# Kernel optimization log

Hardware: AMD Instinct MI355X
Metric: run time of the kernel (lower is better)

The kernel has to match this reference:

```python
import jax, jax.numpy as jnp
import numpy as np

D_MODEL = 1024
NUM_HEADS = 16
HEAD_DIM = D_MODEL // NUM_HEADS
WINDOW = 16
DILATION = 3
SCALE = HEAD_DIM ** -0.5


def _linear(x, W, b):
    # torch nn.Linear: y = x @ W.T + b, W: [out, in]
    return x @ W.T + b


def _chunk_attention(x, Wq, bq, Wk, bk, Wv, bv, chunk):
    B, L, D = x.shape
    pad = (-L) % chunk
    if pad:
        x = jnp.pad(x, ((0, 0), (0, pad), (0, 0)))
    Lp = L + pad
    nC = Lp // chunk
    xr = x.reshape(B * nC, chunk, D)  # [BC, c, D]

    def heads(t):
        return t.reshape(B * nC, chunk, NUM_HEADS, HEAD_DIM).transpose(0, 2, 1, 3)

    q = heads(_linear(xr, Wq, bq))  # [BC, H, c, hd]
    k = heads(_linear(xr, Wk, bk))
    v = heads(_linear(xr, Wv, bv))
    attn = jax.nn.softmax(jnp.einsum('bhqd,bhkd->bhqk', q, k) * SCALE, axis=-1)
    out = jnp.einsum('bhqk,bhkd->bhqd', attn, v)  # [BC, H, c, hd]
    out = out.transpose(0, 2, 1, 3).reshape(B, Lp, D)
    return out[:, :L, :]


def setup_inputs() -> dict:
    key = jax.random.key(0)
    ks = jax.random.split(key, 9)
    s = 1.0 / np.sqrt(D_MODEL)
    x = jax.random.normal(ks[0], (4, 4096, D_MODEL), dtype=jnp.float32)
    def lin(kw, kb):
        W = jax.random.uniform(kw, (D_MODEL, D_MODEL), minval=-s, maxval=s, dtype=jnp.float32)
        b = jax.random.uniform(kb, (D_MODEL,), minval=-s, maxval=s, dtype=jnp.float32)
        return W, b
    Wq, bq = lin(ks[1], ks[2])
    Wk, bk = lin(ks[3], ks[4])
    Wv, bv = lin(ks[5], ks[6])
    Wo, bo = lin(ks[7], ks[8])
    return {"x": x, "Wq": Wq, "bq": bq, "Wk": Wk, "bk": bk,
            "Wv": Wv, "bv": bv, "Wo": Wo, "bo": bo}


def reference(x, Wq, bq, Wk, bk, Wv, bv, Wo, bo):
    B, L, D = x.shape
    # local windowed attention
    local_out = _chunk_attention(x, Wq, bq, Wk, bk, Wv, bv, WINDOW)
    # dilated (atrous) attention: stride-DILATION interleave via reshape/permute
    pad = (-L) % DILATION
    x_pad = jnp.pad(x, ((0, 0), (0, pad), (0, 0))) if pad else x
    Lp = L + pad
    xv = x_pad.reshape(B, Lp // DILATION, DILATION, D).transpose(0, 2, 1, 3)
    x_atrous = xv.reshape(B * DILATION, Lp // DILATION, D)
    a = _chunk_attention(x_atrous, Wq, bq, Wk, bk, Wv, bv, WINDOW)
    a = a.reshape(B, DILATION, Lp // DILATION, D).transpose(0, 2, 1, 3).reshape(B, Lp, D)
    atrous_out = a[:, :L, :]
    return _linear(local_out + atrous_out, Wo, bo)
```

## Files before the change

kernel.cpp:

```cpp
#include <hip/hip_runtime.h>
#include <hip/hip_bf16.h>
#include <stdint.h>

typedef unsigned short ushort_t;
typedef __attribute__((ext_vector_type(8))) short bf16x8;
typedef __attribute__((ext_vector_type(4))) float f32x4;

__device__ __forceinline__ ushort_t f2bf(float f) {
    uint32_t u = __builtin_bit_cast(uint32_t, f);
    u += 0x7FFF + ((u >> 16) & 1);
    return (ushort_t)(u >> 16);
}
__device__ __forceinline__ float bf2f(ushort_t h) {
    return __builtin_bit_cast(float, (uint32_t)h << 16);
}

__device__ __forceinline__ f32x4 mfma16(bf16x8 a, bf16x8 b, f32x4 c) {
    return __builtin_amdgcn_mfma_f32_16x16x32_bf16(a, b, c, 0, 0, 0);
}

#define GLL(g, l) __builtin_amdgcn_global_load_lds(                              \
    (const __attribute__((address_space(1))) void*)(g),                          \
    (__attribute__((address_space(3))) void*)(l), 16, 0, 0)


__global__ __launch_bounds__(256) void cvt_f32_to_bf16(
    const float* __restrict__ src, ushort_t* __restrict__ dst, int n8)
{
    int i = blockIdx.x * blockDim.x + threadIdx.x;
    if (i >= n8) return;
    const float4* s = (const float4*)src + (size_t)i * 2;
    float4 a = s[0], b = s[1];
    union { bf16x8 v; ushort_t u[8]; } o;
    o.u[0] = f2bf(a.x); o.u[1] = f2bf(a.y); o.u[2] = f2bf(a.z); o.u[3] = f2bf(a.w);
    o.u[4] = f2bf(b.x); o.u[5] = f2bf(b.y); o.u[6] = f2bf(b.z); o.u[7] = f2bf(b.w);
    *(bf16x8*)(dst + (size_t)i * 8) = o.v;
}

__global__ __launch_bounds__(256) void pack_bias(
    const float* __restrict__ bq, const float* __restrict__ bk,
    const float* __restrict__ bv, float* __restrict__ dst)
{
    int i = blockIdx.x * blockDim.x + threadIdx.x;
    float v = (i < 1024) ? bq[i] : (i < 2048 ? bk[i - 1024] : bv[i - 2048]);
    dst[i] = v;
}


template<int MODE>
__global__ __launch_bounds__(256) void gemm_bt(
    const ushort_t* __restrict__ A, const ushort_t* __restrict__ B,
    const float* __restrict__ bias, void* __restrict__ outp,
    int M, int K)
{
    __shared__ ushort_t As[128 * 32];
    __shared__ ushort_t Bs[128 * 32];
    const int t = threadIdx.x;
    const int wave = t >> 6, lane = t & 63;
    const int m0 = blockIdx.x * 128;
    const int n0 = blockIdx.y * 128;
    const int wr = wave >> 1, wc = wave & 1;
    const int lg = lane >> 4, ln = lane & 15;

    f32x4 acc[4][4];
#pragma unroll
    for (int i = 0; i < 4; ++i)
#pragma unroll
        for (int j = 0; j < 4; ++j) acc[i][j] = (f32x4){0.f, 0.f, 0.f, 0.f};

    for (int k0 = 0; k0 < K; k0 += 32) {
#pragma unroll
        for (int i = 0; i < 2; ++i) {
            int chunk = i * 256 + t;
            int row = chunk >> 2, kc = chunk & 3;
            const ushort_t* ga = A + (size_t)(m0 + row) * K + (k0 + kc * 8);
            GLL(ga, (char*)As + (i * 256 + wave * 64) * 16);
            const ushort_t* gb = B + (size_t)(n0 + row) * K + (k0 + kc * 8);
            GLL(gb, (char*)Bs + (i * 256 + wave * 64) * 16);
        }
        __syncthreads();
        bf16x8 af[4], bfr[4];
#pragma unroll
        for (int mi = 0; mi < 4; ++mi)
            af[mi] = *(const bf16x8*)&As[(wr * 64 + mi * 16 + ln) * 32 + lg * 8];
#pragma unroll
        for (int ni = 0; ni < 4; ++ni)
            bfr[ni] = *(const bf16x8*)&Bs[(wc * 64 + ni * 16 + ln) * 32 + lg * 8];
#pragma unroll
        for (int mi = 0; mi < 4; ++mi)
#pragma unroll
            for (int ni = 0; ni < 4; ++ni)
                acc[mi][ni] = mfma16(af[mi], bfr[ni], acc[mi][ni]);
        __syncthreads();
    }

#pragma unroll
    for (int mi = 0; mi < 4; ++mi) {
#pragma unroll
        for (int ni = 0; ni < 4; ++ni) {
            int n = n0 + wc * 64 + ni * 16 + ln;
            float bval = bias[n];
#pragma unroll
            for (int r = 0; r < 4; ++r) {
                int m = m0 + wr * 64 + mi * 16 + lg * 4 + r;
                float v = acc[mi][ni][r] + bval;
                if (MODE == 0) {
                    int which = n >> 10, col = n & 1023;
                    ushort_t* o = (ushort_t*)outp + (size_t)which * ((size_t)M * 1024)
                                  + (size_t)m * 1024 + col;
                    *o = f2bf(v);
                } else {
                    ((float*)outp)[(size_t)m * 1024 + n] = v;
                }
            }
        }
    }
}


__device__ __forceinline__ bf16x8 bias8(const float* __restrict__ b, int off) {
    float4 f0 = *(const float4*)(b + off);
    float4 f1 = *(const float4*)(b + off + 4);
    union { bf16x8 v; ushort_t u[8]; } o;
    o.u[0] = f2bf(f0.x); o.u[1] = f2bf(f0.y); o.u[2] = f2bf(f0.z); o.u[3] = f2bf(f0.w);
    o.u[4] = f2bf(f1.x); o.u[5] = f2bf(f1.y); o.u[6] = f2bf(f1.z); o.u[7] = f2bf(f1.w);
    return o.v;
}


__global__ __launch_bounds__(64) void attn_local(
    const ushort_t* __restrict__ Q, const ushort_t* __restrict__ K,
    const ushort_t* __restrict__ V, ushort_t* __restrict__ S)
{
    const int bid = blockIdx.x;
    const int h = bid & 15;
    const int c = bid >> 4;
    const int lane = threadIdx.x;
    const int g = lane >> 4, nn = lane & 15;
    __shared__ ushort_t lds_p[16 * 16];
    __shared__ ushort_t vt[64 * 16];

    const size_t rowb = (size_t)c * 16;
    size_t aoff = (rowb + nn) * 1024 + h * 64 + g * 8;
    bf16x8 qa0 = *(const bf16x8*)(Q + aoff);
    bf16x8 qa1 = *(const bf16x8*)(Q + aoff + 32);
    bf16x8 kb0 = *(const bf16x8*)(K + aoff);
    bf16x8 kb1 = *(const bf16x8*)(K + aoff + 32);
    f32x4 sc = {0.f, 0.f, 0.f, 0.f};
    sc = mfma16(qa0, kb0, sc);
    sc = mfma16(qa1, kb1, sc);

#pragma unroll
    for (int r = 0; r < 4; ++r) {
        float s = sc[r] * 0.125f;
        float mx = s;
#pragma unroll
        for (int off = 1; off < 16; off <<= 1) mx = fmaxf(mx, __shfl_xor(mx, off, 64));
        float e = __expf(s - mx);
        float sm = e;
#pragma unroll
        for (int off = 1; off < 16; off <<= 1) sm += __shfl_xor(sm, off, 64);
        lds_p[(g * 4 + r) * 16 + nn] = f2bf(e / sm);
    }

#pragma unroll
    for (int it = 0; it < 2; ++it) {
        int u = it * 64 + lane;
        int n = u >> 3, cc = u & 7;
        bf16x8 vv = *(const bf16x8*)(V + (rowb + n) * 1024 + h * 64 + cc * 8);
        union { bf16x8 v; ushort_t u8[8]; } vu; vu.v = vv;
#pragma unroll
        for (int j = 0; j < 8; ++j) vt[(cc * 8 + j) * 16 + n] = vu.u8[j];
    }
    __syncthreads();

    bf16x8 zero8 = {};
    bf16x8 pa = (g < 2) ? *(const bf16x8*)&lds_p[nn * 16 + g * 8] : zero8;
#pragma unroll
    for (int dt = 0; dt < 4; ++dt) {
        bf16x8 vb = (g < 2) ? *(const bf16x8*)&vt[(dt * 16 + nn) * 16 + g * 8] : zero8;
        f32x4 o = mfma16(pa, vb, (f32x4){0.f, 0.f, 0.f, 0.f});
#pragma unroll
        for (int r = 0; r < 4; ++r) {
            size_t orow = rowb + g * 4 + r;
            S[orow * 1024 + h * 64 + dt * 16 + nn] = f2bf(o[r]);
        }
    }
}


__global__ __launch_bounds__(64) void attn_atrous(
    const ushort_t* __restrict__ Q, const ushort_t* __restrict__ K,
    const ushort_t* __restrict__ V,
    const float* __restrict__ bq, const float* __restrict__ bk,
    const float* __restrict__ bv, ushort_t* __restrict__ S)
{
    const int bid = blockIdx.x;
    const int h = bid & 15;
    const int tmp = bid >> 4;
    const int c = tmp % 86;
    const int sidx = tmp / 86;
    const int b = sidx / 3, dil = sidx % 3;
    const int lane = threadIdx.x;
    const int g = lane >> 4, nn = lane & 15;
    __shared__ ushort_t lds_p[16 * 16];
    __shared__ ushort_t vt[64 * 16];

    const int dof = h * 64 + g * 8;
    const int p_n = 3 * (c * 16 + nn) + dil;
    bf16x8 qa0, qa1, kb0, kb1;
    if (p_n < 4096) {
        size_t o = ((size_t)b * 4096 + p_n) * 1024 + dof;
        qa0 = *(const bf16x8*)(Q + o);
        qa1 = *(const bf16x8*)(Q + o + 32);
        kb0 = *(const bf16x8*)(K + o);
        kb1 = *(const bf16x8*)(K + o + 32);
    } else {
        qa0 = bias8(bq, dof); qa1 = bias8(bq, dof + 32);
        kb0 = bias8(bk, dof); kb1 = bias8(bk, dof + 32);
    }
    f32x4 sc = {0.f, 0.f, 0.f, 0.f};
    sc = mfma16(qa0, kb0, sc);
    sc = mfma16(qa1, kb1, sc);

#pragma unroll
    for (int r = 0; r < 4; ++r) {
        float s = sc[r] * 0.125f;
        float mx = s;
#pragma unroll
        for (int off = 1; off < 16; off <<= 1) mx = fmaxf(mx, __shfl_xor(mx, off, 64));
        float e = __expf(s - mx);
        float sm = e;
#pragma unroll
        for (int off = 1; off < 16; off <<= 1) sm += __shfl_xor(sm, off, 64);
        lds_p[(g * 4 + r) * 16 + nn] = f2bf(e / sm);
    }

#pragma unroll
    for (int it = 0; it < 2; ++it) {
        int u = it * 64 + lane;
        int n = u >> 3, cc = u & 7;
        int p_v = 3 * (c * 16 + n) + dil;
        bf16x8 vv = (p_v < 4096)
            ? *(const bf16x8*)(V + ((size_t)b * 4096 + p_v) * 1024 + h * 64 + cc * 8)
            : bias8(bv, h * 64 + cc * 8);
        union { bf16x8 v; ushort_t u8[8]; } vu; vu.v = vv;
#pragma unroll
        for (int j = 0; j < 8; ++j) vt[(cc * 8 + j) * 16 + n] = vu.u8[j];
    }
    __syncthreads();

    bf16x8 zero8 = {};
    bf16x8 pa = (g < 2) ? *(const bf16x8*)&lds_p[nn * 16 + g * 8] : zero8;
#pragma unroll
    for (int dt = 0; dt < 4; ++dt) {
        bf16x8 vb = (g < 2) ? *(const bf16x8*)&vt[(dt * 16 + nn) * 16 + g * 8] : zero8;
        f32x4 o = mfma16(pa, vb, (f32x4){0.f, 0.f, 0.f, 0.f});
#pragma unroll
        for (int r = 0; r < 4; ++r) {
            int p_q = 3 * (c * 16 + g * 4 + r) + dil;
            if (p_q < 4096) {
                size_t off = ((size_t)b * 4096 + p_q) * 1024 + h * 64 + dt * 16 + nn;
                S[off] = f2bf(bf2f(S[off]) + o[r]);
            }
        }
    }
}


extern "C" void kernel_launch(void* const* d_in, const int* in_sizes, int n_in,
                              void* d_out, int out_size, void* d_ws, size_t ws_size,
                              hipStream_t stream)
{
    const float* x  = (const float*)d_in[0];
    const float* Wq = (const float*)d_in[1];
    const float* bq = (const float*)d_in[2];
    const float* Wk = (const float*)d_in[3];
    const float* bk = (const float*)d_in[4];
    const float* Wv = (const float*)d_in[5];
    const float* bv = (const float*)d_in[6];
    const float* Wo = (const float*)d_in[7];
    const float* bo = (const float*)d_in[8];
    float* out = (float*)d_out;

    const size_t NT = 16384;
    ushort_t* xb   = (ushort_t*)d_ws;
    ushort_t* wqkv = xb + NT * 1024;
    ushort_t* wo   = wqkv + 3 * 1024 * 1024;
    ushort_t* Qb   = wo + 1024 * 1024;
    ushort_t* Kb   = Qb + NT * 1024;
    ushort_t* Vb   = Kb + NT * 1024;
    ushort_t* Sb   = Vb + NT * 1024;
    float*    bqkv = (float*)(Sb + NT * 1024);

    const int n8x = (int)(NT * 1024 / 8);
    cvt_f32_to_bf16<<<n8x / 256, 256, 0, stream>>>(x, xb, n8x);
    const int n8w = 1024 * 1024 / 8;
    cvt_f32_to_bf16<<<n8w / 256, 256, 0, stream>>>(Wq, wqkv,               n8w);
    cvt_f32_to_bf16<<<n8w / 256, 256, 0, stream>>>(Wk, wqkv + 1024 * 1024, n8w);
    cvt_f32_to_bf16<<<n8w / 256, 256, 0, stream>>>(Wv, wqkv + 2 * 1024 * 1024, n8w);
    cvt_f32_to_bf16<<<n8w / 256, 256, 0, stream>>>(Wo, wo, n8w);
    pack_bias<<<12, 256, 0, stream>>>(bq, bk, bv, bqkv);

    gemm_bt<0><<<dim3(128, 24), 256, 0, stream>>>(xb, wqkv, bqkv, (void*)Qb, (int)NT, 1024);

    attn_local <<<16384, 64, 0, stream>>>(Qb, Kb, Vb, Sb);
    attn_atrous<<<16512, 64, 0, stream>>>(Qb, Kb, Vb, bq, bk, bv, Sb);

    gemm_bt<1><<<dim3(128, 8), 256, 0, stream>>>(Sb, wo, bo, (void*)out, (int)NT, 1024);
}
```

Before: 423.3 us.

## Fuse conversion kernels, add triple-buffered swizzled GEMM, pack attention waves per block

Merges the six conversion and bias-packing launches into one kernel. Replaces the 128x128 single-buffered GEMM with a 256x128-tile, 512-thread GEMM that uses a 3-stage LDS ring, XOR-swizzled LDS layout, split prefetch, raised wave priority around the MFMA blocks, and a grid swizzle for L2 locality. The two attention kernels now run four independent 64-lane units per 256-thread block instead of one per block. The changes target launch overhead, GEMM memory latency and LDS bank conflicts, and block scheduling cost. In exchange they use much more LDS per block and add more complex hand-written wait-count and barrier logic.

```diff
diff --git a/kernel.cpp b/kernel.cpp
--- a/kernel.cpp
+++ b/kernel.cpp
@@ -23,43 +23,74 @@
     (const __attribute__((address_space(1))) void*)(g),                          \
     (__attribute__((address_space(3))) void*)(l), 16, 0, 0)
 
-
-__global__ __launch_bounds__(256) void cvt_f32_to_bf16(
-    const float* __restrict__ src, ushort_t* __restrict__ dst, int n8)
-{
-    int i = blockIdx.x * blockDim.x + threadIdx.x;
-    if (i >= n8) return;
-    const float4* s = (const float4*)src + (size_t)i * 2;
-    float4 a = s[0], b = s[1];
+#define CFENCE asm volatile("" ::: "memory")
+#define BARRIER do { CFENCE; __builtin_amdgcn_s_barrier(); CFENCE; } while (0)
+
+
+__device__ __forceinline__ void cvt8(const float* s, ushort_t* d) {
+    float4 a = ((const float4*)s)[0], b = ((const float4*)s)[1];
     union { bf16x8 v; ushort_t u[8]; } o;
     o.u[0] = f2bf(a.x); o.u[1] = f2bf(a.y); o.u[2] = f2bf(a.z); o.u[3] = f2bf(a.w);
     o.u[4] = f2bf(b.x); o.u[5] = f2bf(b.y); o.u[6] = f2bf(b.z); o.u[7] = f2bf(b.w);
-    *(bf16x8*)(dst + (size_t)i * 8) = o.v;
-}
-
-__global__ __launch_bounds__(256) void pack_bias(
+    *(bf16x8*)d = o.v;
+}
+
+__global__ __launch_bounds__(256) void cvt_all(
+    const float* __restrict__ x,
+    const float* __restrict__ Wq, const float* __restrict__ Wk,
+    const float* __restrict__ Wv, const float* __restrict__ Wo,
     const float* __restrict__ bq, const float* __restrict__ bk,
-    const float* __restrict__ bv, float* __restrict__ dst)
-{
-    int i = blockIdx.x * blockDim.x + threadIdx.x;
-    float v = (i < 1024) ? bq[i] : (i < 2048 ? bk[i - 1024] : bv[i - 2048]);
-    dst[i] = v;
-}
-
+    const float* __restrict__ bv,
+    ushort_t* __restrict__ xb, ushort_t* __restrict__ wqkv,
+    float* __restrict__ bqkv)
+{
+    const int NX = 16384 * 1024 / 8;
+    const int NW = 1024 * 1024 / 8;
+    int i = blockIdx.x * 256 + threadIdx.x;
+    if (i < NX) {
+        cvt8(x + (size_t)i * 8, xb + (size_t)i * 8);
+    } else if (i < NX + 4 * NW) {
+        int j = i - NX;
+        int w = j >> 17, off = j & (NW - 1);
+        const float* s = (w == 0) ? Wq : (w == 1) ? Wk : (w == 2) ? Wv : Wo;
+        cvt8(s + (size_t)off * 8, wqkv + (size_t)j * 8);
+    } else if (i < NX + 4 * NW + 384) {
+        int j = i - NX - 4 * NW;
+        int w2 = j >> 7, off = j & 127;
+        const float* s = (w2 == 0) ? bq : (w2 == 1) ? bk : bv;
+        ((float4*)(bqkv + j * 8))[0] = ((const float4*)(s + off * 8))[0];
+        ((float4*)(bqkv + j * 8))[1] = ((const float4*)(s + off * 8))[1];
+    }
+}
+
+
+#define STAGE_A(jj)  { int idx = (jj) * 512 + tid; int row = idx >> 3, ch = idx & 7;    \
+    GLL(A + (size_t)(m0 + row) * 1024 + kt2 * 64 + ((ch ^ (row & 7)) * 8),             \
+        (char*)Abn + (size_t)idx * 16); }
+#define STAGE_B(jj)  { int idx = (jj) * 512 + tid; int row = idx >> 3, ch = idx & 7;    \
+    GLL(B + (size_t)(n0 + row) * 1024 + kt2 * 64 + ((ch ^ (row & 7)) * 8),             \
+        (char*)Bbn + (size_t)idx * 16); }
 
 template<int MODE>
-__global__ __launch_bounds__(256) void gemm_bt(
+__global__ __launch_bounds__(512, 2) void gemm3(
     const ushort_t* __restrict__ A, const ushort_t* __restrict__ B,
     const float* __restrict__ bias, void* __restrict__ outp,
-    int M, int K)
-{
-    __shared__ ushort_t As[128 * 32];
-    __shared__ ushort_t Bs[128 * 32];
-    const int t = threadIdx.x;
-    const int wave = t >> 6, lane = t & 63;
-    const int m0 = blockIdx.x * 128;
-    const int n0 = blockIdx.y * 128;
-    const int wr = wave >> 1, wc = wave & 1;
+    int M, int NTN)
+{
+    __shared__ ushort_t As[3][256 * 64];
+    __shared__ ushort_t Bs[3][128 * 64];
+    const int NK = 16;
+
+    const int nwg = gridDim.x;
+    const int bid = blockIdx.x;
+    const int q8 = nwg >> 3;
+    const int swz = (bid & 7) * q8 + (bid >> 3);
+    const int m0 = (swz / NTN) * 256;
+    const int n0 = (swz % NTN) * 128;
+
+    const int tid = threadIdx.x;
+    const int wave = tid >> 6, lane = tid & 63;
+    const int wm = wave >> 1, wn = wave & 1;
     const int lg = lane >> 4, ln = lane & 15;
 
     f32x4 acc[4][4];
@@ -68,47 +99,94 @@
 #pragma unroll
         for (int j = 0; j < 4; ++j) acc[i][j] = (f32x4){0.f, 0.f, 0.f, 0.f};
 
-    for (int k0 = 0; k0 < K; k0 += 32) {
-#pragma unroll
-        for (int i = 0; i < 2; ++i) {
-            int chunk = i * 256 + t;
-            int row = chunk >> 2, kc = chunk & 3;
-            const ushort_t* ga = A + (size_t)(m0 + row) * K + (k0 + kc * 8);
-            GLL(ga, (char*)As + (i * 256 + wave * 64) * 16);
-            const ushort_t* gb = B + (size_t)(n0 + row) * K + (k0 + kc * 8);
-            GLL(gb, (char*)Bs + (i * 256 + wave * 64) * 16);
-        }
-        __syncthreads();
-        bf16x8 af[4], bfr[4];
+    {
+        ushort_t* Abn = &As[0][0]; ushort_t* Bbn = &Bs[0][0]; int kt2 = 0;
+        STAGE_A(0) STAGE_A(1) STAGE_A(2) STAGE_A(3) STAGE_B(0) STAGE_B(1)
+    }
+    {
+        ushort_t* Abn = &As[1][0]; ushort_t* Bbn = &Bs[1][0]; int kt2 = 1;
+        STAGE_A(0) STAGE_A(1) STAGE_A(2) STAGE_A(3) STAGE_B(0) STAGE_B(1)
+    }
+    asm volatile("s_waitcnt vmcnt(6)" ::: "memory");
+    BARRIER;
+
+    int bc = 0;
+    for (int kt = 0; kt < NK; ++kt) {
+        int bn = bc + 2; if (bn >= 3) bn -= 3;
+        const ushort_t* Ab = &As[bc][0];
+        const ushort_t* Bb = &Bs[bc][0];
+        ushort_t* Abn = &As[bn][0];
+        ushort_t* Bbn = &Bs[bn][0];
+        const int kt2 = kt + 2;
+        const bool pf = (kt2 < NK);
+
+        bf16x8 af[4][2], b01[2][2];
+#pragma unroll
+        for (int mi = 0; mi < 4; ++mi) {
+            int row = wm * 64 + mi * 16 + ln;
+#pragma unroll
+            for (int kk = 0; kk < 2; ++kk)
+                af[mi][kk] = *(const bf16x8*)&Ab[row * 64 + (((kk * 4 + lg) ^ (row & 7)) * 8)];
+        }
+#pragma unroll
+        for (int ni = 0; ni < 2; ++ni) {
+            int row = wn * 64 + ni * 16 + ln;
+#pragma unroll
+            for (int kk = 0; kk < 2; ++kk)
+                b01[ni][kk] = *(const bf16x8*)&Bb[row * 64 + (((kk * 4 + lg) ^ (row & 7)) * 8)];
+        }
+        if (pf) { STAGE_A(0) STAGE_A(1) STAGE_A(2) }
+        BARRIER;
+        __builtin_amdgcn_s_setprio(1);
 #pragma unroll
         for (int mi = 0; mi < 4; ++mi)
-            af[mi] = *(const bf16x8*)&As[(wr * 64 + mi * 16 + ln) * 32 + lg * 8];
-#pragma unroll
-        for (int ni = 0; ni < 4; ++ni)
-            bfr[ni] = *(const bf16x8*)&Bs[(wc * 64 + ni * 16 + ln) * 32 + lg * 8];
+#pragma unroll
+            for (int ni = 0; ni < 2; ++ni) {
+                acc[mi][ni] = mfma16(af[mi][0], b01[ni][0], acc[mi][ni]);
+                acc[mi][ni] = mfma16(af[mi][1], b01[ni][1], acc[mi][ni]);
+            }
+        __builtin_amdgcn_s_setprio(0);
+
+        bf16x8 b23[2][2];
+#pragma unroll
+        for (int ni = 0; ni < 2; ++ni) {
+            int row = wn * 64 + (ni + 2) * 16 + ln;
+#pragma unroll
+            for (int kk = 0; kk < 2; ++kk)
+                b23[ni][kk] = *(const bf16x8*)&Bb[row * 64 + (((kk * 4 + lg) ^ (row & 7)) * 8)];
+        }
+        if (pf) { STAGE_A(3) STAGE_B(0) STAGE_B(1) }
+        BARRIER;
+        __builtin_amdgcn_s_setprio(1);
 #pragma unroll
         for (int mi = 0; mi < 4; ++mi)
 #pragma unroll
-            for (int ni = 0; ni < 4; ++ni)
-                acc[mi][ni] = mfma16(af[mi], bfr[ni], acc[mi][ni]);
-        __syncthreads();
-    }
-
-#pragma unroll
-    for (int mi = 0; mi < 4; ++mi) {
-#pragma unroll
-        for (int ni = 0; ni < 4; ++ni) {
-            int n = n0 + wc * 64 + ni * 16 + ln;
-            float bval = bias[n];
+            for (int ni = 0; ni < 2; ++ni) {
+                acc[mi][ni + 2] = mfma16(af[mi][0], b23[ni][0], acc[mi][ni + 2]);
+                acc[mi][ni + 2] = mfma16(af[mi][1], b23[ni][1], acc[mi][ni + 2]);
+            }
+        __builtin_amdgcn_s_setprio(0);
+
+        if (pf) { asm volatile("s_waitcnt vmcnt(6)" ::: "memory"); }
+        else    { asm volatile("s_waitcnt vmcnt(0)" ::: "memory"); }
+        BARRIER;
+        bc += 1; if (bc == 3) bc = 0;
+    }
+
+#pragma unroll
+    for (int ni = 0; ni < 4; ++ni) {
+        int n = n0 + wn * 64 + ni * 16 + ln;
+        float bval = bias[n];
+#pragma unroll
+        for (int mi = 0; mi < 4; ++mi) {
 #pragma unroll
             for (int r = 0; r < 4; ++r) {
-                int m = m0 + wr * 64 + mi * 16 + lg * 4 + r;
+                int m = m0 + wm * 64 + mi * 16 + lg * 4 + r;
                 float v = acc[mi][ni][r] + bval;
                 if (MODE == 0) {
                     int which = n >> 10, col = n & 1023;
-                    ushort_t* o = (ushort_t*)outp + (size_t)which * ((size_t)M * 1024)
-                                  + (size_t)m * 1024 + col;
-                    *o = f2bf(v);
+                    ((ushort_t*)outp)[(size_t)which * ((size_t)M * 1024)
+                                      + (size_t)m * 1024 + col] = f2bf(v);
                 } else {
                     ((float*)outp)[(size_t)m * 1024 + n] = v;
                 }
@@ -128,17 +206,17 @@
 }
 
 
-__global__ __launch_bounds__(64) void attn_local(
+__global__ __launch_bounds__(256) void attn_local(
     const ushort_t* __restrict__ Q, const ushort_t* __restrict__ K,
     const ushort_t* __restrict__ V, ushort_t* __restrict__ S)
 {
-    const int bid = blockIdx.x;
-    const int h = bid & 15;
-    const int c = bid >> 4;
-    const int lane = threadIdx.x;
+    const int wave = threadIdx.x >> 6, lane = threadIdx.x & 63;
+    const int unit = blockIdx.x * 4 + wave;
+    const int h = unit & 15;
+    const int c = unit >> 4;
     const int g = lane >> 4, nn = lane & 15;
-    __shared__ ushort_t lds_p[16 * 16];
-    __shared__ ushort_t vt[64 * 16];
+    __shared__ ushort_t lds_p[4][16 * 16];
+    __shared__ ushort_t vt[4][64 * 16];
 
     const size_t rowb = (size_t)c * 16;
     size_t aoff = (rowb + nn) * 1024 + h * 64 + g * 8;
@@ -160,7 +238,7 @@
         float sm = e;
 #pragma unroll
         for (int off = 1; off < 16; off <<= 1) sm += __shfl_xor(sm, off, 64);
-        lds_p[(g * 4 + r) * 16 + nn] = f2bf(e / sm);
+        lds_p[wave][(g * 4 + r) * 16 + nn] = f2bf(e / sm);
     }
 
 #pragma unroll
@@ -170,15 +248,15 @@
         bf16x8 vv = *(const bf16x8*)(V + (rowb + n) * 1024 + h * 64 + cc * 8);
         union { bf16x8 v; ushort_t u8[8]; } vu; vu.v = vv;
 #pragma unroll
-        for (int j = 0; j < 8; ++j) vt[(cc * 8 + j) * 16 + n] = vu.u8[j];
+        for (int j = 0; j < 8; ++j) vt[wave][(cc * 8 + j) * 16 + n] = vu.u8[j];
     }
     __syncthreads();
 
     bf16x8 zero8 = {};
-    bf16x8 pa = (g < 2) ? *(const bf16x8*)&lds_p[nn * 16 + g * 8] : zero8;
+    bf16x8 pa = (g < 2) ? *(const bf16x8*)&lds_p[wave][nn * 16 + g * 8] : zero8;
 #pragma unroll
     for (int dt = 0; dt < 4; ++dt) {
-        bf16x8 vb = (g < 2) ? *(const bf16x8*)&vt[(dt * 16 + nn) * 16 + g * 8] : zero8;
+        bf16x8 vb = (g < 2) ? *(const bf16x8*)&vt[wave][(dt * 16 + nn) * 16 + g * 8] : zero8;
         f32x4 o = mfma16(pa, vb, (f32x4){0.f, 0.f, 0.f, 0.f});
 #pragma unroll
         for (int r = 0; r < 4; ++r) {
@@ -189,22 +267,22 @@
 }
 
 
-__global__ __launch_bounds__(64) void attn_atrous(
+__global__ __launch_bounds__(256) void attn_atrous(
     const ushort_t* __restrict__ Q, const ushort_t* __restrict__ K,
     const ushort_t* __restrict__ V,
     const float* __restrict__ bq, const float* __restrict__ bk,
     const float* __restrict__ bv, ushort_t* __restrict__ S)
 {
-    const int bid = blockIdx.x;
-    const int h = bid & 15;
-    const int tmp = bid >> 4;
+    const int wave = threadIdx.x >> 6, lane = threadIdx.x & 63;
+    const int unit = blockIdx.x * 4 + wave;
+    const int h = unit & 15;
+    const int tmp = unit >> 4;
     const int c = tmp % 86;
     const int sidx = tmp / 86;
     const int b = sidx / 3, dil = sidx % 3;
-    const int lane = threadIdx.x;
     const int g = lane >> 4, nn = lane & 15;
-    __shared__ ushort_t lds_p[16 * 16];
-    __shared__ ushort_t vt[64 * 16];
+    __shared__ ushort_t lds_p[4][16 * 16];
+    __shared__ ushort_t vt[4][64 * 16];
 
     const int dof = h * 64 + g * 8;
     const int p_n = 3 * (c * 16 + nn) + dil;
@@ -233,7 +311,7 @@
         float sm = e;
 #pragma unroll
         for (int off = 1; off < 16; off <<= 1) sm += __shfl_xor(sm, off, 64);
-        lds_p[(g * 4 + r) * 16 + nn] = f2bf(e / sm);
+        lds_p[wave][(g * 4 + r) * 16 + nn] = f2bf(e / sm);
     }
 
 #pragma unroll
@@ -246,15 +324,15 @@
             : bias8(bv, h * 64 + cc * 8);
         union { bf16x8 v; ushort_t u8[8]; } vu; vu.v = vv;
 #pragma unroll
-        for (int j = 0; j < 8; ++j) vt[(cc * 8 + j) * 16 + n] = vu.u8[j];
+        for (int j = 0; j < 8; ++j) vt[wave][(cc * 8 + j) * 16 + n] = vu.u8[j];
     }
     __syncthreads();
 
     bf16x8 zero8 = {};
-    bf16x8 pa = (g < 2) ? *(const bf16x8*)&lds_p[nn * 16 + g * 8] : zero8;
+    bf16x8 pa = (g < 2) ? *(const bf16x8*)&lds_p[wave][nn * 16 + g * 8] : zero8;
 #pragma unroll
     for (int dt = 0; dt < 4; ++dt) {
-        bf16x8 vb = (g < 2) ? *(const bf16x8*)&vt[(dt * 16 + nn) * 16 + g * 8] : zero8;
+        bf16x8 vb = (g < 2) ? *(const bf16x8*)&vt[wave][(dt * 16 + nn) * 16 + g * 8] : zero8;
         f32x4 o = mfma16(pa, vb, (f32x4){0.f, 0.f, 0.f, 0.f});
 #pragma unroll
         for (int r = 0; r < 4; ++r) {
@@ -293,19 +371,14 @@
     ushort_t* Sb   = Vb + NT * 1024;
     float*    bqkv = (float*)(Sb + NT * 1024);
 
-    const int n8x = (int)(NT * 1024 / 8);
-    cvt_f32_to_bf16<<<n8x / 256, 256, 0, stream>>>(x, xb, n8x);
-    const int n8w = 1024 * 1024 / 8;
-    cvt_f32_to_bf16<<<n8w / 256, 256, 0, stream>>>(Wq, wqkv,               n8w);
-    cvt_f32_to_bf16<<<n8w / 256, 256, 0, stream>>>(Wk, wqkv + 1024 * 1024, n8w);
-    cvt_f32_to_bf16<<<n8w / 256, 256, 0, stream>>>(Wv, wqkv + 2 * 1024 * 1024, n8w);
-    cvt_f32_to_bf16<<<n8w / 256, 256, 0, stream>>>(Wo, wo, n8w);
-    pack_bias<<<12, 256, 0, stream>>>(bq, bk, bv, bqkv);
-
-    gemm_bt<0><<<dim3(128, 24), 256, 0, stream>>>(xb, wqkv, bqkv, (void*)Qb, (int)NT, 1024);
-
-    attn_local <<<16384, 64, 0, stream>>>(Qb, Kb, Vb, Sb);
-    attn_atrous<<<16512, 64, 0, stream>>>(Qb, Kb, Vb, bq, bk, bv, Sb);
-
-    gemm_bt<1><<<dim3(128, 8), 256, 0, stream>>>(Sb, wo, bo, (void*)out, (int)NT, 1024);
-}
+    const int total_units = 2097152 + 4 * 131072 + 384;
+    cvt_all<<<(total_units + 255) / 256, 256, 0, stream>>>(
+        x, Wq, Wk, Wv, Wo, bq, bk, bv, xb, wqkv, bqkv);
+
+    gemm3<0><<<1536, 512, 0, stream>>>(xb, wqkv, bqkv, (void*)Qb, (int)NT, 24);
+
+    attn_local <<<4096, 256, 0, stream>>>(Qb, Kb, Vb, Sb);
+    attn_atrous<<<4128, 256, 0, stream>>>(Qb, Kb, Vb, bq, bk, bv, Sb);
+
+    gemm3<1><<<512, 512, 0, stream>>>(Sb, wo, bo, (void*)out, (int)NT, 8);
+}
```

Measured after the change: 368.4 us. 13.0% less time.
